# Kernel optimization log

Measured on AMD Instinct MI355X. Metric: run time of the kernel, lower is better.

The kernel has to match this reference:

```python
import jax, jax.numpy as jnp
import numpy as np

COST_W = {'cls': 1.0, 'center': 0.0, 'obj_ness': 0.0, 'giou': 2.0}
IOU_THRES = 0.25
MAX_DYN = 10
EPS = 1e-6
N_PRED, N_GT, N_CLS = 65536, 128, 256


def _to_bbox(centers, sizes):
    # center/size -> (x1,y1,z1,x2,y2,z2)
    return jnp.concatenate([centers - sizes / 2.0, centers + sizes / 2.0], axis=-1)


def _giou_3d(b1, b2):
    # b1 [N,6], b2 [M,6] -> giou [N,M] (axis_aligned_bbox_overlaps_3d, mode='giou')
    vol1 = jnp.prod(b1[:, 3:] - b1[:, :3], axis=-1)  # [N]
    vol2 = jnp.prod(b2[:, 3:] - b2[:, :3], axis=-1)  # [M]
    lt = jnp.maximum(b1[:, None, :3], b2[None, :, :3])  # [N,M,3]
    rb = jnp.minimum(b1[:, None, 3:], b2[None, :, 3:])
    overlap = jnp.prod(jnp.clip(rb - lt, 0.0), axis=-1)  # [N,M]
    union = jnp.maximum(vol1[:, None] + vol2[None, :] - overlap, EPS)
    iou = overlap / union
    elt = jnp.minimum(b1[:, None, :3], b2[None, :, :3])
    erb = jnp.maximum(b1[:, None, 3:], b2[None, :, 3:])
    enclose = jnp.maximum(jnp.prod(jnp.clip(erb - elt, 0.0), axis=-1), EPS)
    return iou - (enclose - union) / enclose


def _lsa(cost):
    # Jonker-Volgenant shortest-augmenting-path LAP (same optimum as
    # scipy.optimize.linear_sum_assignment). cost [n, m], n <= m.
    # Returns col4row[n]: column matched to each row.
    n, m = cost.shape
    u = np.zeros(n, np.float64)
    v = np.zeros(m, np.float64)
    col4row = np.full(n, -1, np.int64)
    row4col = np.full(m, -1, np.int64)
    cost = cost.astype(np.float64)
    for cur in range(n):
        shortest = np.full(m, np.inf)
        path = np.full(m, -1, np.int64)
        SC = np.zeros(m, bool)
        SR = []
        i, min_val, sink = cur, 0.0, -1
        while sink == -1:
            SR.append(i)
            r = min_val + cost[i] - u[i] - v
            upd = (~SC) & (r < shortest)
            shortest = np.where(upd, r, shortest)
            path = np.where(upd, i, path)
            masked = np.where(SC, np.inf, shortest)
            j = int(masked.argmin())
            min_val = masked[j]
            SC[j] = True
            if row4col[j] == -1:
                sink = j
            else:
                i = int(row4col[j])
        u[cur] += min_val
        for i2 in SR:
            if i2 != cur:
                u[i2] += min_val - shortest[col4row[i2]]
        v[SC] -= min_val - shortest[SC]
        j = sink
        while True:
            i2 = int(path[j])
            row4col[j] = i2
            col4row[i2], j = j, col4row[i2]
            if i2 == cur:
                break
    return col4row


def _dynamic_assign(giou, used0, order):
    # Sequential greedy IoU-threshold assignment over gts (ascending max-iou).
    NEG = jnp.float32(-1e9)
    n_pred = giou.shape[0]

    def step(used, gt_idx):
        col = giou[:, gt_idx]
        vals = jnp.where((col > IOU_THRES) & (~used), col, NEG)
        topv, topi = jax.lax.top_k(vals, MAX_DYN)
        valid = topv > NEG
        used = used | jnp.zeros((n_pred,), bool).at[topi].set(valid)
        return used, (jnp.where(valid, topi, -1), jnp.where(valid, gt_idx, -1))

    _, (dp, dg) = jax.lax.scan(step, used0, order)
    return dp.reshape(-1), dg.reshape(-1)  # padded with -1 where invalid


def setup_inputs() -> dict:
    key = jax.random.key(0)
    k = jax.random.split(key, 7)
    return {
        'all_centers': jax.random.normal(k[0], (N_PRED, 3), jnp.float32),
        'all_sizes': jax.random.uniform(k[1], (N_PRED, 3), jnp.float32),
        'all_cls': jax.random.normal(k[2], (N_PRED, N_CLS), jnp.float32),
        'all_objness': jax.random.normal(k[3], (N_PRED,), jnp.float32),
        'gt_centers': jax.random.normal(k[4], (N_GT, 3), jnp.float32),
        'gt_sizes': jax.random.uniform(k[5], (N_GT, 3), jnp.float32),
        'gt_labels': jax.random.randint(k[6], (N_GT,), 0, N_CLS, jnp.int64),
    }


def reference(all_centers, all_sizes, all_cls, all_objness, gt_centers, gt_sizes, gt_labels):
    pred_bbox = _to_bbox(all_centers, all_sizes)
    gt_bbox = _to_bbox(gt_centers, gt_sizes)
    giou = _giou_3d(pred_bbox, gt_bbox)  # [N, M]
    cost_class = -jax.nn.sigmoid(all_cls)[:, gt_labels]  # [N, M]
    cost_center = jnp.sum(jnp.abs(all_centers[:, None, :] - gt_centers[None, :, :]), axis=-1)  # cdist p=1
    cost_obj = -jax.nn.sigmoid(all_objness)[:, None]  # [N, 1]
    total_cost = (COST_W['cls'] * cost_class + COST_W['center'] * cost_center
                  + COST_W['obj_ness'] * cost_obj + COST_W['giou'] * (-giou))
    # Hungarian on transposed cost (M <= N): same optimal pairing as scipy on [N, M].
    col4row = _lsa(np.asarray(jax.device_get(total_cost)).T)
    pred_indices = jnp.asarray(col4row, jnp.int64)       # matched pred per gt
    gt_indices = jnp.arange(gt_labels.shape[0], dtype=jnp.int64)
    used0 = jnp.zeros((giou.shape[0],), bool).at[pred_indices].set(True)
    order = jnp.argsort(jnp.max(giou, axis=0))
    dp, dg = _dynamic_assign(giou, used0, order)
    combined_preds = jnp.concatenate([pred_indices, dp.astype(jnp.int64)])
    combined_gts = jnp.concatenate([gt_indices, dg.astype(jnp.int64)])
    return combined_preds, combined_gts
```

## Files before the change

### kernel.cpp

```cpp
#include <hip/hip_runtime.h>
#include <hip/hip_bf16.h>
#include <math.h>

#define NPRED 65536
#define NGT   128
#define NCLS  256
#define CAP   12288
#define VCAP  160
#define VSLOT 129
#define NLIST 129
#define LSTRIDE 132
#define KEEP  2048
#define KMIN  1418
#define GSPLIT 4
#define GPB   (NGT / GSPLIT)
#define SENT_I 0x7FFFFFFF


__device__ __forceinline__ unsigned f2u(float f) {
    unsigned u = __float_as_uint(f);
    return (u & 0x80000000u) ? ~u : (u | 0x80000000u);
}
__device__ __forceinline__ float u2f(unsigned x) {
    unsigned u = (x & 0x80000000u) ? (x ^ 0x80000000u) : ~x;
    return __uint_as_float(u);
}
__device__ __forceinline__ unsigned long long d2u(double d) {
    unsigned long long u = (unsigned long long)__double_as_longlong(d);
    return (u & 0x8000000000000000ull) ? ~u : (u | 0x8000000000000000ull);
}
__device__ __forceinline__ double u2d(unsigned long long x) {
    unsigned long long u = (x & 0x8000000000000000ull) ? (x ^ 0x8000000000000000ull) : ~x;
    return __longlong_as_double((long long)u);
}

__device__ __forceinline__ float giou3d(
    float pl0, float pl1, float pl2, float ph0, float ph1, float ph2, float pvol,
    float gl0, float gl1, float gl2, float gh0, float gh1, float gh2, float gvol)
{
#pragma clang fp contract(off)
    float c0 = fmaxf(fminf(ph0, gh0) - fmaxf(pl0, gl0), 0.0f);
    float c1 = fmaxf(fminf(ph1, gh1) - fmaxf(pl1, gl1), 0.0f);
    float c2 = fmaxf(fminf(ph2, gh2) - fmaxf(pl2, gl2), 0.0f);
    float overlap = (c0 * c1) * c2;
    float uni = fmaxf((pvol + gvol) - overlap, 1e-6f);
    float iou = overlap / uni;
    float e0 = fmaxf(fmaxf(ph0, gh0) - fminf(pl0, gl0), 0.0f);
    float e1 = fmaxf(fmaxf(ph1, gh1) - fminf(pl1, gl1), 0.0f);
    float e2 = fmaxf(fmaxf(ph2, gh2) - fminf(pl2, gl2), 0.0f);
    float enc = fmaxf((e0 * e1) * e2, 1e-6f);
    return iou - (enc - uni) / enc;
}


__global__ __launch_bounds__(256) void k_gather(
    const float* __restrict__ cls, const int* __restrict__ lab,
    float* __restrict__ costT,
    int* __restrict__ ccnt, unsigned* __restrict__ cmax, int* __restrict__ failFlag)
{
#pragma clang fp contract(off)
    __shared__ float tile[64][NCLS + 1];
    __shared__ int labl[NGT];
    int tid = threadIdx.x;
    int p0 = blockIdx.x * 64;
    if (blockIdx.x == 0) {
        if (tid < NGT) { ccnt[tid] = 0; cmax[tid] = 0u; }
        if (tid == 0) *failFlag = 0;
    }
    if (tid < NGT) labl[tid] = lab[tid];
    for (int it = 0; it < 16; ++it) {
        int row = it * 4 + (tid >> 6);
        int col = (tid & 63) * 4;
        const float4 v = *(const float4*)&cls[(size_t)(p0 + row) * NCLS + col];
        tile[row][col + 0] = v.x; tile[row][col + 1] = v.y;
        tile[row][col + 2] = v.z; tile[row][col + 3] = v.w;
    }
    __syncthreads();
    int lane = tid & 63;
    for (int rep = 0; rep < 32; ++rep) {
        int g = rep * 4 + (tid >> 6);
        float val = tile[lane][labl[g]];
        double s = 1.0 / (1.0 + exp(-(double)val));
        costT[(size_t)g * NPRED + p0 + lane] = -(float)s;
    }
}

__global__ __launch_bounds__(256) void k_cost(
    const float* __restrict__ pc, const float* __restrict__ ps,
    const float* __restrict__ gc, const float* __restrict__ gs,
    float* __restrict__ costT, int* __restrict__ ccnt, unsigned* __restrict__ cmax,
    int2* __restrict__ cpair)
{
#pragma clang fp contract(off)
    __shared__ float gb[GPB][6];
    __shared__ float gvol[GPB];
    __shared__ unsigned smax[GPB];
    __shared__ int cntl[GPB], basel[GPB], curl[GPB];
    int tid = threadIdx.x;
    int lane = tid & 63;
    int g0 = (blockIdx.x & (GSPLIT - 1)) * GPB;
    int p  = (blockIdx.x >> 2) * 256 + tid;

    if (tid < GPB) {
        int g = g0 + tid;
        float c0 = gc[g * 3 + 0], c1 = gc[g * 3 + 1], c2 = gc[g * 3 + 2];
        float s0 = gs[g * 3 + 0], s1 = gs[g * 3 + 1], s2 = gs[g * 3 + 2];
        float l0 = c0 - s0 / 2.0f, l1 = c1 - s1 / 2.0f, l2 = c2 - s2 / 2.0f;
        float h0 = c0 + s0 / 2.0f, h1 = c1 + s1 / 2.0f, h2 = c2 + s2 / 2.0f;
        gb[tid][0] = l0; gb[tid][1] = l1; gb[tid][2] = l2;
        gb[tid][3] = h0; gb[tid][4] = h1; gb[tid][5] = h2;
        gvol[tid] = ((h0 - l0) * (h1 - l1)) * (h2 - l2);
        smax[tid] = 0u; cntl[tid] = 0; curl[tid] = 0;
    }
    __syncthreads();

    float c0 = pc[p * 3 + 0], c1 = pc[p * 3 + 1], c2 = pc[p * 3 + 2];
    float s0 = ps[p * 3 + 0], s1 = ps[p * 3 + 1], s2 = ps[p * 3 + 2];
    float pl0 = c0 - s0 / 2.0f, pl1 = c1 - s1 / 2.0f, pl2 = c2 - s2 / 2.0f;
    float ph0 = c0 + s0 / 2.0f, ph1 = c1 + s1 / 2.0f, ph2 = c2 + s2 / 2.0f;
    float pvol = ((ph0 - pl0) * (ph1 - pl1)) * (ph2 - pl2);

    float gior[GPB];

#pragma unroll
    for (int gg = 0; gg < GPB; ++gg) {
        float gio = giou3d(pl0, pl1, pl2, ph0, ph1, ph2, pvol,
                           gb[gg][0], gb[gg][1], gb[gg][2], gb[gg][3], gb[gg][4], gb[gg][5],
                           gvol[gg]);
        gior[gg] = gio;
        float m = gio;
        for (int off = 32; off; off >>= 1) m = fmaxf(m, __shfl_xor(m, off, 64));
        unsigned long long mask = __ballot(gio > 0.25f);
        if (lane == 0) {
            atomicMax(&smax[gg], f2u(m));
            atomicAdd(&cntl[gg], __popcll(mask));
        }
        size_t ij = (size_t)(g0 + gg) * NPRED + p;
        float ns = costT[ij];
        costT[ij] = ns + (2.0f * (-gio));
    }
    __syncthreads();
    if (tid < GPB) {
        atomicMax(&cmax[g0 + tid], smax[tid]);
        basel[tid] = atomicAdd(&ccnt[g0 + tid], cntl[tid]);
    }
    __syncthreads();

#pragma unroll
    for (int gg = 0; gg < GPB; ++gg) {
        float gio = gior[gg];
        bool cand = (gio > 0.25f);
        unsigned long long mask = __ballot(cand);
        int cnt = __popcll(mask);
        int wo = 0;
        if (lane == 0 && cnt) wo = atomicAdd(&curl[gg], cnt);
        wo = __shfl(wo, 0, 64);
        if (cand) {
            int slot = basel[gg] + wo + __popcll(mask & ((1ull << lane) - 1ull));
            if (slot < CAP)
                cpair[(size_t)(g0 + gg) * CAP + slot] = make_int2(p, __float_as_int(gio));
        }
    }
}

__global__ __launch_bounds__(256) void k_toprow(
    const float* __restrict__ costT, int2* __restrict__ rowlist,
    const unsigned* __restrict__ cmax, int* __restrict__ order)
{
    __shared__ unsigned long long keys[2048];
    __shared__ int hist[256];
    __shared__ unsigned long long sh_prefix;
    __shared__ int sh_rank, sh_cnt, sh_ok;
    __shared__ unsigned msort[NGT];
    int tid = threadIdx.x;
    int row = blockIdx.x;

    if (row == NGT) {
        if (tid < NGT) msort[tid] = cmax[tid];
        __syncthreads();
        if (tid < NGT) {
            unsigned mt = msort[tid];
            int r = 0;
            for (int k = 0; k < NGT; ++k) {
                unsigned mk = msort[k];
                if (mk < mt || (mk == mt && k < tid)) r++;
            }
            order[r] = tid;
        }
        return;
    }
    const float* crow = costT + (size_t)row * NPRED;

    unsigned long long lv[8];
#pragma unroll
    for (int q = 0; q < 8; ++q) lv[q] = ~0ull;
    const float4* crow4 = (const float4*)crow;
    for (int it = tid; it < NPRED / 4; it += 256) {
        float4 v4 = crow4[it];
        int j = it * 4;
        float vv[4] = {v4.x, v4.y, v4.z, v4.w};
#pragma unroll
        for (int e = 0; e < 4; ++e) {
            unsigned long long key =
                ((unsigned long long)f2u(vv[e]) << 32) | (unsigned)(j + e);
            if (key < lv[7]) {
                unsigned long long c = key;
#pragma unroll
                for (int q = 0; q < 8; ++q) {
                    unsigned long long mx = (c > lv[q]) ? c : lv[q];
                    unsigned long long mn = (c > lv[q]) ? lv[q] : c;
                    lv[q] = mn; c = mx;
                }
            }
        }
    }
#pragma unroll
    for (int q = 0; q < 8; ++q) keys[tid * 8 + q] = lv[q];
    if (tid == 0) sh_ok = 1;
    __syncthreads();

    for (int k = 2; k <= 2048; k <<= 1) {
        for (int j2 = k >> 1; j2 > 0; j2 >>= 1) {
            for (int i = tid; i < 2048; i += 256) {
                int ixj = i ^ j2;
                if (ixj > i) {
                    unsigned long long a = keys[i], b2 = keys[ixj];
                    bool up = ((i & k) == 0);
                    if ((up && a > b2) || (!up && a < b2)) { keys[i] = b2; keys[ixj] = a; }
                }
            }
            __syncthreads();
        }
    }

    unsigned long long thr = keys[NLIST - 1];
    if (lv[7] < thr) sh_ok = 0;
    __syncthreads();

    if (sh_ok) {
        if (tid < NLIST) {
            unsigned long long key = keys[tid];
            rowlist[row * LSTRIDE + tid] =
                make_int2(__float_as_int(u2f((unsigned)(key >> 32))),
                          (int)(unsigned)(key & 0xFFFFFFFFull));
        }
        return;
    }

    if (tid == 0) { sh_prefix = 0ull; sh_rank = NLIST - 1; sh_cnt = 0; }
    __syncthreads();
    for (int d = 7; d >= 0; --d) {
        hist[tid] = 0;
        __syncthreads();
        unsigned long long pref = sh_prefix;
        int sh = (d + 1) * 8;
        for (int j = tid; j < NPRED; j += 256) {
            unsigned long long key = ((unsigned long long)f2u(crow[j]) << 32) | (unsigned)j;
            bool match = (sh >= 64) || ((key >> sh) == (pref >> sh));
            if (match) atomicAdd(&hist[(int)((key >> (d * 8)) & 255ull)], 1);
        }
        __syncthreads();
        if (tid == 0) {
            int rank = sh_rank, cum = 0, b = 0;
            for (; b < 256; ++b) { if (cum + hist[b] > rank) break; cum += hist[b]; }
            sh_prefix = pref | ((unsigned long long)b << (d * 8));
            sh_rank = rank - cum;
        }
        __syncthreads();
    }
    unsigned long long thr2 = sh_prefix;
    for (int j = tid; j < NPRED; j += 256) {
        unsigned long long key = ((unsigned long long)f2u(crow[j]) << 32) | (unsigned)j;
        if (key <= thr2) { int s = atomicAdd(&sh_cnt, 1); keys[s] = key; }
    }
    __syncthreads();
    if (tid >= sh_cnt) keys[tid] = ~0ull;
    __syncthreads();
    for (int k = 2; k <= 256; k <<= 1) {
        for (int j2 = k >> 1; j2 > 0; j2 >>= 1) {
            int i = tid, ixj = i ^ j2;
            if (ixj > i) {
                unsigned long long a = keys[i], b2 = keys[ixj];
                bool up = ((i & k) == 0);
                if ((up && a > b2) || (!up && a < b2)) { keys[i] = b2; keys[ixj] = a; }
            }
            __syncthreads();
        }
    }
    if (tid < NLIST) {
        unsigned long long key = keys[tid];
        rowlist[row * LSTRIDE + tid] =
            make_int2(__float_as_int(u2f((unsigned)(key >> 32))),
                      (int)(unsigned)(key & 0xFFFFFFFFull));
    }
}

__global__ __launch_bounds__(64) void k_lsa_sparse(
    const float* __restrict__ costT, const int2* __restrict__ rowlist,
    int* __restrict__ failFlag,
    unsigned* __restrict__ usedbits, int* __restrict__ out)
{
#pragma clang fp contract(off)
    __shared__ float  costV[NGT][VSLOT];
    __shared__ double u_l[NGT];
    __shared__ int    c4r[NGT];
    __shared__ int    slot4row[NGT];
    __shared__ int    headpos[NGT];
    __shared__ int    colidV[VCAP];
    __shared__ int    pathV[VCAP], r4cV[VCAP];
    __shared__ int    SRr[VCAP];
    __shared__ double headv[VCAP];
    __shared__ int    headj[VCAP];
    __shared__ unsigned vbits[2048];

    int lane = threadIdx.x;
    for (int w = lane; w < 2048; w += 64) vbits[w] = 0u;
    for (int r = lane; r < NGT; r += 64) {
        u_l[r] = 0.0; c4r[r] = -1; slot4row[r] = -1; headpos[r] = 0;
    }
    double short0 = INFINITY, short1 = INFINITY;
    double v0 = 0.0, v1 = 0.0;
    int col0 = SENT_I, col1 = SENT_I;
    int sc0 = 0, sc1 = 0;
    int nV = 0;
    bool fail = false;
    __syncthreads();

    for (int cur = 0; cur < NGT && !fail; ++cur) {
        short0 = INFINITY; short1 = INFINITY; sc0 = 0; sc1 = 0;
        if (lane < nV)      pathV[lane]      = -1;
        if (lane + 64 < nV) pathV[lane + 64] = -1;
        if (lane == 0) SRr[0] = cur;
        int bi = cur, s = 1, pendrow = cur, pendpos = 0, sink = -1;
        double mv = 0.0, pendmv = 0.0;
        __syncthreads();
        int pos = headpos[cur];
        int i0 = pos + lane;
        int2 e0 = (i0 < NLIST) ? rowlist[cur * LSTRIDE + i0] : make_int2(0, SENT_I);

        while (true) {
            int prow = pendrow;
            int pp   = pendpos;
            double pmv = pendmv;

            double ui = u_l[bi];
            unsigned long long bvk = ~0ull, btk = ~0ull;
            if (lane < nV && !sc0) {
                double c = (double)costV[bi][lane];
                double r = ((mv + c) - ui) - v0;
                if (r < short0) { short0 = r; pathV[lane] = bi; }
                unsigned long long vk = d2u(short0);
                unsigned long long tk = ((unsigned long long)(unsigned)col0 << 32)
                                        | (0x80000000u | (unsigned)lane);
                if (vk < bvk || (vk == bvk && tk < btk)) { bvk = vk; btk = tk; }
            }
            int k1 = lane + 64;
            if (k1 < nV && !sc1) {
                double c = (double)costV[bi][k1];
                double r = ((mv + c) - ui) - v1;
                if (r < short1) { short1 = r; pathV[k1] = bi; }
                unsigned long long vk = d2u(short1);
                unsigned long long tk = ((unsigned long long)(unsigned)col1 << 32)
                                        | (0x80000000u | (unsigned)k1);
                if (vk < bvk || (vk == bvk && tk < btk)) { bvk = vk; btk = tk; }
            }
            for (int p = lane; p < s; p += 64) {
                if (p == pp) continue;
                unsigned long long vk = d2u(headv[p]);
                unsigned long long tk = ((unsigned long long)(unsigned)headj[p] << 32)
                                        | (unsigned)p;
                if (vk < bvk || (vk == bvk && tk < btk)) { bvk = vk; btk = tk; }
            }

            int hcol = SENT_I; float hval = 0.0f;
            {
                int c0 = e0.y;
                bool fresh = (i0 < NLIST) && !((vbits[c0 >> 5] >> (c0 & 31)) & 1u);
                unsigned long long m0 = __ballot(fresh);
                if (m0) {
                    int fl = __ffsll(m0) - 1;
                    hcol = __shfl(c0, fl, 64);
                    hval = __shfl(__int_as_float(e0.x), fl, 64);
                    pos += fl;
                } else {
                    pos += 64;
                    while (pos < NLIST) {
                        int i = pos + lane;
                        int2 e = (i < NLIST) ? rowlist[prow * LSTRIDE + i] : make_int2(0, SENT_I);
                        int c = e.y;
                        bool fr = (i < NLIST) && !((vbits[c >> 5] >> (c & 31)) & 1u);
                        unsigned long long m = __ballot(fr);
                        if (m) {
                            int fl = __ffsll(m) - 1;
                            hcol = __shfl(c, fl, 64);
                            hval = __shfl(__int_as_float(e.x), fl, 64);
                            pos += fl;
                            break;
                        }
                        pos += 64;
                    }
                }
            }
            double pend_headv = (hcol == SENT_I) ? (double)INFINITY
                                : ((pmv + (double)hval) - u_l[prow]);
            {
                unsigned long long vk = d2u(pend_headv);
                unsigned long long tk = ((unsigned long long)(unsigned)hcol << 32)
                                        | (unsigned)pp;
                if (vk < bvk || (vk == bvk && tk < btk)) { bvk = vk; btk = tk; }
            }

#pragma unroll
            for (int off = 1; off < 64; off <<= 1) {
                unsigned long long ov = __shfl_xor(bvk, off, 64);
                unsigned long long ot = __shfl_xor(btk, off, 64);
                if (ov < bvk || (ov == bvk && ot < btk)) { bvk = ov; btk = ot; }
            }
            double bv = u2d(bvk);
            unsigned tlow = (unsigned)btk;
            int bj   = (int)(btk >> 32);
            int bisv = (int)(tlow >> 31);
            int baux = (int)(tlow & 0x7FFFFFFFu);
            mv = bv;

            if (lane == 0) {
                headpos[prow] = pos;
                headv[pp] = pend_headv; headj[pp] = hcol;
            }
            if (bisv) {
                if ((baux & 63) == lane) {
                    if (baux & 64) sc1 = 1; else sc0 = 1;
                }
                int nr = r4cV[baux];
                if (lane == 0) SRr[s] = nr;
                pendrow = nr; pendpos = s; pendmv = bv; bi = nr; ++s;
                pos = headpos[nr];
                i0 = pos + lane;
                e0 = (i0 < NLIST) ? rowlist[nr * LSTRIDE + i0] : make_int2(0, SENT_I);
                __syncthreads();
            } else {
                if (nV >= VCAP) {
                    fail = true;
                } else {
                    if ((nV & 63) == lane) {
                        if (nV & 64) { col1 = bj; v1 = 0.0; short1 = bv; sc1 = 1; }
                        else         { col0 = bj; v0 = 0.0; short0 = bv; sc0 = 1; }
                    }
                    if (lane == 0) {
                        colidV[nV] = bj;
                        pathV[nV] = SRr[baux]; r4cV[nV] = -1;
                        vbits[bj >> 5] |= (1u << (bj & 31));
                    }
                    sink = bj;
                    ++nV;
                }
                __syncthreads();
                break;
            }
        }
        if (fail) break;

        int snew = nV - 1;
        float pfa = costT[(size_t)lane * NPRED + sink];
        float pfb = costT[(size_t)(lane + 64) * NPRED + sink];

        double mvf = mv;
        if (lane < nV && sc0)      v0 -= (mvf - short0);
        if (lane + 64 < nV && sc1) v1 -= (mvf - short1);

        {
            int q = lane;
            bool act = (q >= 1 && q < s);
            int i2 = act ? SRr[q] : 0;
            int sl = act ? slot4row[i2] : 0;
            double gA = __shfl(short0, sl & 63, 64);
            double gB = __shfl(short1, sl & 63, 64);
            double sv = (sl & 64) ? gB : gA;
            if (act) u_l[i2] += mvf - sv;
        }
        {
            int q = lane + 64;
            bool act = (q >= 1 && q < s);
            int i2 = act ? SRr[q] : 0;
            int sl = act ? slot4row[i2] : 0;
            double gA = __shfl(short0, sl & 63, 64);
            double gB = __shfl(short1, sl & 63, 64);
            double sv = (sl & 64) ? gB : gA;
            if (act) u_l[i2] += mvf - sv;
        }
        if (lane == 0) u_l[cur] += mvf;

        if (lane == 0) {
            int jslot = snew;
            while (true) {
                int i2 = pathV[jslot];
                r4cV[jslot] = i2;
                int oldslot = (c4r[i2] >= 0) ? slot4row[i2] : -1;
                c4r[i2] = colidV[jslot];
                slot4row[i2] = jslot;
                if (i2 == cur) break;
                jslot = oldslot;
            }
        }
        costV[lane][snew]      = pfa;
        costV[lane + 64][snew] = pfb;
        __syncthreads();
    }

    if (lane == 0 && fail) *failFlag = 1;
    __syncthreads();
    if (!fail) {
        for (int w = lane; w < 2048; w += 64) usedbits[w] = 0u;
        __syncthreads();
        for (int r = lane; r < NGT; r += 64) {
            int p = c4r[r];
            atomicOr(&usedbits[p >> 5], 1u << (p & 31));
            out[r] = p;
            out[1408 + r] = r;
        }
    }
}

__global__ __launch_bounds__(1024) void k_lsa_dense(
    const float* __restrict__ costT, const int* __restrict__ failFlag,
    double* __restrict__ v, double* __restrict__ shortest,
    int* __restrict__ path, int* __restrict__ row4col,
    unsigned char* __restrict__ SC, unsigned* __restrict__ usedbits,
    int* __restrict__ out)
{
#pragma clang fp contract(off)
    if (*failFlag == 0) return;
    __shared__ double u_l[NGT];
    __shared__ int    c4r[NGT];
    __shared__ int    SR[NGT + 1];
    __shared__ int    bi, bsink, nSR;
    __shared__ double bmin;
    __shared__ double wval[16];
    __shared__ int    widx[16];
    int tid = threadIdx.x;

    for (int j = tid; j < NPRED; j += 1024) { v[j] = 0.0; row4col[j] = -1; }
    if (tid < NGT) { u_l[tid] = 0.0; c4r[tid] = -1; }
    __syncthreads();

    for (int cur = 0; cur < NGT; ++cur) {
        for (int j = tid; j < NPRED; j += 1024) {
            shortest[j] = (double)INFINITY; path[j] = -1; SC[j] = 0;
        }
        if (tid == 0) { bi = cur; bsink = -1; bmin = 0.0; SR[0] = cur; nSR = 1; }
        __syncthreads();

        while (true) {
            int irow = bi;
            double mv = bmin;
            double ui = u_l[irow];
            const float* crow = costT + (size_t)irow * NPRED;
            double bestv = (double)INFINITY;
            int    bestj = SENT_I;
            for (int j = tid; j < NPRED; j += 1024) {
                if (!SC[j]) {
                    double s = shortest[j];
                    double r = ((mv + (double)crow[j]) - ui) - v[j];
                    if (r < s) { s = r; shortest[j] = r; path[j] = irow; }
                    if (s < bestv || (s == bestv && j < bestj)) { bestv = s; bestj = j; }
                }
            }
            for (int off = 32; off; off >>= 1) {
                double ov = __shfl_down(bestv, off, 64);
                int    oj = __shfl_down(bestj, off, 64);
                if (ov < bestv || (ov == bestv && oj < bestj)) { bestv = ov; bestj = oj; }
            }
            if ((tid & 63) == 0) { wval[tid >> 6] = bestv; widx[tid >> 6] = bestj; }
            __syncthreads();
            if (tid == 0) {
                double bv = wval[0]; int bj = widx[0];
                for (int w = 1; w < 16; ++w) {
                    double ov = wval[w]; int oj = widx[w];
                    if (ov < bv || (ov == bv && oj < bj)) { bv = ov; bj = oj; }
                }
                bmin = bv;
                SC[bj] = 1;
                int r = row4col[bj];
                if (r < 0) { bsink = bj; }
                else       { SR[nSR++] = r; bi = r; }
            }
            __syncthreads();
            if (bsink >= 0) break;
        }

        double mv = bmin;
        for (int j = tid; j < NPRED; j += 1024)
            if (SC[j]) v[j] -= (mv - shortest[j]);
        if (tid == 0) {
            u_l[cur] += mv;
            for (int k = 1; k < nSR; ++k) {
                int i2 = SR[k];
                u_l[i2] += mv - shortest[c4r[i2]];
            }
            int j = bsink;
            while (true) {
                int i2 = path[j];
                row4col[j] = i2;
                int nj = c4r[i2];
                c4r[i2] = j;
                j = nj;
                if (i2 == cur) break;
            }
        }
        __syncthreads();
    }

    for (int w = tid; w < 2048; w += 1024) usedbits[w] = 0u;
    __syncthreads();
    for (int j = tid; j < NPRED; j += 1024)
        if (row4col[j] >= 0) atomicOr(&usedbits[j >> 5], 1u << (j & 31));
    if (tid < NGT) {
        out[tid]        = c4r[tid];
        out[1408 + tid] = tid;
    }
}

__global__ __launch_bounds__(256) void k_prep(
    const int2* __restrict__ cpair, const int* __restrict__ ccnt,
    unsigned long long* __restrict__ scand, int* __restrict__ kcount,
    int* __restrict__ fullflag)
{
    __shared__ int hist[256];
    __shared__ unsigned long long keys[KEEP];
    __shared__ unsigned sh_pref, sh_thresh;
    __shared__ int sh_done, sh_fail, sh_cnt;
    int tid = threadIdx.x;
    int g = blockIdx.x;
    int nc = ccnt[g]; if (nc > CAP) nc = CAP;
    const int2* src = cpair + (size_t)g * CAP;

    unsigned thresh = 0;
    if (nc > KEEP - 1) {
        if (tid == 0) { sh_pref = 0; sh_done = 0; sh_fail = 0; }
        __syncthreads();
        int above = 0;
        for (int byt = 3; byt >= 0; --byt) {
            hist[tid] = 0;
            __syncthreads();
            unsigned pref = sh_pref;
            for (int c = tid; c < nc; c += 256) {
                unsigned u = f2u(__int_as_float(src[c].y));
                if (byt == 3 || (u >> ((byt + 1) * 8)) == (pref >> ((byt + 1) * 8)))
                    atomicAdd(&hist[(u >> (byt * 8)) & 255], 1);
            }
            __syncthreads();
            if (tid == 0) {
                int cum = 0, B = 0, kept = 0, abnew = above;
                for (int b = 255; b >= 0; --b) {
                    if (above + cum + hist[b] >= KMIN) {
                        B = b; kept = above + cum + hist[b]; abnew = above + cum; break;
                    }
                    cum += hist[b];
                }
                if (kept <= KEEP - 1) { sh_thresh = sh_pref | ((unsigned)B << (byt * 8)); sh_done = 1; }
                else {
                    above = abnew;
                    sh_pref = sh_pref | ((unsigned)B << (byt * 8));
                    if (byt == 0) sh_fail = 1;
                }
            }
            __syncthreads();
            if (sh_done || sh_fail) break;
        }
        if (sh_fail) {
            if (tid == 0) { fullflag[g] = 1; kcount[g] = 0; }
            return;
        }
        thresh = sh_thresh;
    }
    if (tid == 0) sh_cnt = 0;
    __syncthreads();
    for (int c = tid; c < nc; c += 256) {
        unsigned u = f2u(__int_as_float(src[c].y));
        if (u >= thresh) {
            int slot = atomicAdd(&sh_cnt, 1);
            keys[slot] = ((unsigned long long)(~u) << 32) | (unsigned)src[c].x;
        }
    }
    __syncthreads();
    int kept = sh_cnt;
    for (int i = tid; i < KEEP; i += 256) if (i >= kept) keys[i] = ~0ull;
    __syncthreads();
    for (int k = 2; k <= KEEP; k <<= 1) {
        for (int j = k >> 1; j > 0; j >>= 1) {
            for (int i = tid; i < KEEP; i += 256) {
                int ixj = i ^ j;
                if (ixj > i) {
                    unsigned long long a = keys[i], b = keys[ixj];
                    bool up = ((i & k) == 0);
                    if ((up && a > b) || (!up && a < b)) { keys[i] = b; keys[ixj] = a; }
                }
            }
            __syncthreads();
        }
    }
    for (int i = tid; i < KEEP; i += 256) scand[(size_t)g * KEEP + i] = keys[i];
    if (tid == 0) { kcount[g] = kept; fullflag[g] = 0; }
}

__global__ __launch_bounds__(64) void k_dyn2(
    const int* __restrict__ order, const int* __restrict__ kcount,
    const unsigned long long* __restrict__ scand, const int* __restrict__ fullflag,
    const int* __restrict__ ccnt, const int2* __restrict__ cpair,
    const unsigned* __restrict__ usedbits_g, const int* __restrict__ failFlag,
    int* __restrict__ out)
{
    __shared__ unsigned bits[2048];
    int lane = threadIdx.x;
    for (int w = lane; w < 2048; w += 64) bits[w] = usedbits_g[w];
    __syncthreads();
    bool globalFull = (*failFlag != 0);

    for (int k = 0; k < NGT; ++k) {
        int gt = order[k];
        int got = 0;
        if (!globalFull && fullflag[gt] == 0) {
            int kept = kcount[gt];
            int base = 0;
            while (got < 10 && base < kept) {
                int i = base + lane;
                unsigned long long key = (i < kept) ? scand[(size_t)gt * KEEP + i] : ~0ull;
                int p = (int)(unsigned)(key & 0xFFFFFFFFull);
                bool ok = (key != ~0ull) && !((bits[p >> 5] >> (p & 31)) & 1u);
                unsigned long long mask = __ballot(ok);
                int need = 10 - got;
                int pre = __popcll(mask & ((1ull << lane) - 1ull));
                if (ok && pre < need) {
                    out[128 + k * 10 + got + pre] = p;
                    out[1408 + 128 + k * 10 + got + pre] = gt;
                    atomicOr(&bits[p >> 5], 1u << (p & 31));
                }
                int tot = __popcll(mask);
                got += (tot < need) ? tot : need;
                base += 64;
                __syncthreads();
            }
        } else {
            int nc = ccnt[gt]; if (nc > CAP) nc = CAP;
            float lv[10]; int li[10];
#pragma unroll
            for (int q = 0; q < 10; ++q) { lv[q] = -1e30f; li[q] = SENT_I; }
            for (int c = lane; c < nc; c += 64) {
                int2 pr = cpair[(size_t)gt * CAP + c];
                int p = pr.x;
                if ((bits[p >> 5] >> (p & 31)) & 1u) continue;
                float cv = __int_as_float(pr.y); int ci = p;
#pragma unroll
                for (int q = 0; q < 10; ++q) {
                    bool b = (cv > lv[q]) || (cv == lv[q] && ci < li[q]);
                    float tv = b ? lv[q] : cv; int ti = b ? li[q] : ci;
                    if (b) { lv[q] = cv; li[q] = ci; }
                    cv = tv; ci = ti;
                }
            }
#pragma unroll
            for (int q = 0; q < 10; ++q) {
                float mo = lv[0]; int mj = li[0];
#pragma unroll
                for (int off = 1; off < 64; off <<= 1) {
                    float ov = __shfl_xor(mo, off, 64);
                    int oj = __shfl_xor(mj, off, 64);
                    if (ov > mo || (ov == mo && oj < mj)) { mo = ov; mj = oj; }
                }
                bool valid = (mj != SENT_I);
                if (valid && li[0] == mj) {
#pragma unroll
                    for (int t = 0; t < 9; ++t) { lv[t] = lv[t + 1]; li[t] = li[t + 1]; }
                    lv[9] = -1e30f; li[9] = SENT_I;
                }
                if (lane == q) {
                    out[128 + k * 10 + q] = valid ? mj : -1;
                    out[1408 + 128 + k * 10 + q] = valid ? gt : -1;
                    if (valid) atomicOr(&bits[mj >> 5], 1u << (mj & 31));
                }
            }
            got = 10;
            __syncthreads();
        }
        for (int q = got + lane; q < 10; q += 64) {
            out[128 + k * 10 + q] = -1;
            out[1408 + 128 + k * 10 + q] = -1;
        }
        __syncthreads();
    }
}


extern "C" void kernel_launch(void* const* d_in, const int* in_sizes, int n_in,
                              void* d_out, int out_size, void* d_ws, size_t ws_size,
                              hipStream_t stream) {
    const float* pc  = (const float*)d_in[0];
    const float* ps  = (const float*)d_in[1];
    const float* cls = (const float*)d_in[2];
    const float* gc  = (const float*)d_in[4];
    const float* gs  = (const float*)d_in[5];
    const int*   lab = (const int*)d_in[6];

    char* ws = (char*)d_ws;
    float*         costT    = (float*)(ws + 0);
    unsigned long long* scand = (unsigned long long*)(ws + 0);
    int2*          rowlist  = (int2*)(ws + 33554432);
    double*        v        = (double*)(ws + 33554432);
    double*        shortest = (double*)(ws + 34078720);
    int*           path     = (int*)(ws + 34603008);
    int*           row4col  = (int*)(ws + 34865152);
    unsigned char* SC       = (unsigned char*)(ws + 35127296);
    int*           kcount   = (int*)(ws + 35192832);
    int*           fullflag = (int*)(ws + 35193344);
    int*           ccnt     = (int*)(ws + 35193856);
    unsigned*      cmax     = (unsigned*)(ws + 35194368);
    int*           order    = (int*)(ws + 35194880);
    int*           failFlag = (int*)(ws + 35195392);
    unsigned*      usedbits = (unsigned*)(ws + 35195904);
    int2*          cpair    = (int2*)(ws + 35204096);

    int* out = (int*)d_out;

    hipLaunchKernelGGL(k_gather, dim3(NPRED / 64), dim3(256), 0, stream,
                       cls, lab, costT, ccnt, cmax, failFlag);
    hipLaunchKernelGGL(k_cost, dim3((NPRED / 256) * GSPLIT), dim3(256), 0, stream,
                       pc, ps, gc, gs, costT, ccnt, cmax, cpair);
    hipLaunchKernelGGL(k_toprow, dim3(NGT + 1), dim3(256), 0, stream,
                       costT, rowlist, cmax, order);
    hipLaunchKernelGGL(k_lsa_sparse, dim3(1), dim3(64), 0, stream,
                       costT, rowlist, failFlag, usedbits, out);
    hipLaunchKernelGGL(k_lsa_dense, dim3(1), dim3(1024), 0, stream,
                       costT, failFlag, v, shortest, path, row4col, SC, usedbits, out);
    hipLaunchKernelGGL(k_prep, dim3(NGT), dim3(256), 0, stream,
                       cpair, ccnt, scand, kcount, fullflag);
    hipLaunchKernelGGL(k_dyn2, dim3(1), dim3(64), 0, stream,
                       order, kcount, scand, fullflag, ccnt, cpair, usedbits, failFlag, out);
}
```

Measured before the change: 690.3 us.

## Replace bitonic sort in top-row selection with radix select over candidates

k_toprow now runs with 512 threads, each keeping its 8 smallest keys, so there are 4096 candidates in shared memory. The full 2048-key bitonic sort is replaced by an 8-pass radix histogram select over those candidates to find the 129th-smallest threshold. Keys at or below the threshold are compacted into a 256-entry buffer, which is then bitonic-sorted. The fallback full-row radix select is kept for the case where a thread's local list may have overflowed. The aim is to cut sort synchronisation and shared-memory traffic in exchange for eight rounds of histogram atomics; with 129 blocks on a large GPU, occupancy and parallelism also change.

```diff
diff --git a/kernel.cpp b/kernel.cpp
--- a/kernel.cpp
+++ b/kernel.cpp
@@ -14,6 +14,7 @@
 #define KMIN  1418
 #define GSPLIT 4
 #define GPB   (NGT / GSPLIT)
+#define NCAND 4096
 #define SENT_I 0x7FFFFFFF
 
 
@@ -163,11 +164,12 @@
     }
 }
 
-__global__ __launch_bounds__(256) void k_toprow(
+__global__ __launch_bounds__(512) void k_toprow(
     const float* __restrict__ costT, int2* __restrict__ rowlist,
     const unsigned* __restrict__ cmax, int* __restrict__ order)
 {
-    __shared__ unsigned long long keys[2048];
+    __shared__ unsigned long long keys[NCAND];
+    __shared__ unsigned long long cbuf[256];
     __shared__ int hist[256];
     __shared__ unsigned long long sh_prefix;
     __shared__ int sh_rank, sh_cnt, sh_ok;
@@ -190,14 +192,12 @@
         return;
     }
     const float* crow = costT + (size_t)row * NPRED;
+    const float4* crow4 = (const float4*)crow;
 
     unsigned long long lv[8];
 #pragma unroll
     for (int q = 0; q < 8; ++q) lv[q] = ~0ull;
-    const float4* crow4 = (const float4*)crow;
-    for (int it = tid; it < NPRED / 4; it += 256) {
-        float4 v4 = crow4[it];
-        int j = it * 4;
+    auto ins4 = [&](float4 v4, int j) {
         float vv[4] = {v4.x, v4.y, v4.z, v4.w};
 #pragma unroll
         for (int e = 0; e < 4; ++e) {
@@ -213,49 +213,29 @@
                 }
             }
         }
+    };
+    for (int base = 0; base < 32; base += 4) {
+        float4 va = crow4[tid + (base + 0) * 512];
+        float4 vb = crow4[tid + (base + 1) * 512];
+        float4 vc = crow4[tid + (base + 2) * 512];
+        float4 vd = crow4[tid + (base + 3) * 512];
+        ins4(va, (tid + (base + 0) * 512) * 4);
+        ins4(vb, (tid + (base + 1) * 512) * 4);
+        ins4(vc, (tid + (base + 2) * 512) * 4);
+        ins4(vd, (tid + (base + 3) * 512) * 4);
     }
 #pragma unroll
     for (int q = 0; q < 8; ++q) keys[tid * 8 + q] = lv[q];
-    if (tid == 0) sh_ok = 1;
-    __syncthreads();
-
-    for (int k = 2; k <= 2048; k <<= 1) {
-        for (int j2 = k >> 1; j2 > 0; j2 >>= 1) {
-            for (int i = tid; i < 2048; i += 256) {
-                int ixj = i ^ j2;
-                if (ixj > i) {
-                    unsigned long long a = keys[i], b2 = keys[ixj];
-                    bool up = ((i & k) == 0);
-                    if ((up && a > b2) || (!up && a < b2)) { keys[i] = b2; keys[ixj] = a; }
-                }
-            }
-            __syncthreads();
-        }
-    }
-
-    unsigned long long thr = keys[NLIST - 1];
-    if (lv[7] < thr) sh_ok = 0;
-    __syncthreads();
-
-    if (sh_ok) {
-        if (tid < NLIST) {
-            unsigned long long key = keys[tid];
-            rowlist[row * LSTRIDE + tid] =
-                make_int2(__float_as_int(u2f((unsigned)(key >> 32))),
-                          (int)(unsigned)(key & 0xFFFFFFFFull));
-        }
-        return;
-    }
-
-    if (tid == 0) { sh_prefix = 0ull; sh_rank = NLIST - 1; sh_cnt = 0; }
-    __syncthreads();
+    if (tid == 0) { sh_ok = 1; sh_prefix = 0ull; sh_rank = NLIST - 1; sh_cnt = 0; }
+    __syncthreads();
+
     for (int d = 7; d >= 0; --d) {
-        hist[tid] = 0;
+        if (tid < 256) hist[tid] = 0;
         __syncthreads();
         unsigned long long pref = sh_prefix;
         int sh = (d + 1) * 8;
-        for (int j = tid; j < NPRED; j += 256) {
-            unsigned long long key = ((unsigned long long)f2u(crow[j]) << 32) | (unsigned)j;
+        for (int i = tid; i < NCAND; i += 512) {
+            unsigned long long key = keys[i];
             bool match = (sh >= 64) || ((key >> sh) == (pref >> sh));
             if (match) atomicAdd(&hist[(int)((key >> (d * 8)) & 255ull)], 1);
         }
@@ -268,27 +248,65 @@
         }
         __syncthreads();
     }
-    unsigned long long thr2 = sh_prefix;
-    for (int j = tid; j < NPRED; j += 256) {
-        unsigned long long key = ((unsigned long long)f2u(crow[j]) << 32) | (unsigned)j;
-        if (key <= thr2) { int s = atomicAdd(&sh_cnt, 1); keys[s] = key; }
-    }
-    __syncthreads();
-    if (tid >= sh_cnt) keys[tid] = ~0ull;
+    unsigned long long t = sh_prefix;
+    if (lv[7] < t) sh_ok = 0;
+    __syncthreads();
+    bool ok = (sh_ok != 0);
+
+    if (ok) {
+        for (int i = tid; i < NCAND; i += 512) {
+            unsigned long long key = keys[i];
+            if (key <= t) { int s2 = atomicAdd(&sh_cnt, 1); cbuf[s2] = key; }
+        }
+        __syncthreads();
+    } else {
+        if (tid == 0) { sh_prefix = 0ull; sh_rank = NLIST - 1; sh_cnt = 0; }
+        __syncthreads();
+        for (int d = 7; d >= 0; --d) {
+            if (tid < 256) hist[tid] = 0;
+            __syncthreads();
+            unsigned long long pref = sh_prefix;
+            int sh = (d + 1) * 8;
+            for (int j = tid; j < NPRED; j += 512) {
+                unsigned long long key = ((unsigned long long)f2u(crow[j]) << 32) | (unsigned)j;
+                bool match = (sh >= 64) || ((key >> sh) == (pref >> sh));
+                if (match) atomicAdd(&hist[(int)((key >> (d * 8)) & 255ull)], 1);
+            }
+            __syncthreads();
+            if (tid == 0) {
+                int rank = sh_rank, cum = 0, b = 0;
+                for (; b < 256; ++b) { if (cum + hist[b] > rank) break; cum += hist[b]; }
+                sh_prefix = pref | ((unsigned long long)b << (d * 8));
+                sh_rank = rank - cum;
+            }
+            __syncthreads();
+        }
+        unsigned long long thr2 = sh_prefix;
+        for (int j = tid; j < NPRED; j += 512) {
+            unsigned long long key = ((unsigned long long)f2u(crow[j]) << 32) | (unsigned)j;
+            if (key <= thr2) { int s2 = atomicAdd(&sh_cnt, 1); cbuf[s2] = key; }
+        }
+        __syncthreads();
+    }
+
+    int kept = sh_cnt;
+    if (tid < 256 && tid >= kept) cbuf[tid] = ~0ull;
     __syncthreads();
     for (int k = 2; k <= 256; k <<= 1) {
         for (int j2 = k >> 1; j2 > 0; j2 >>= 1) {
-            int i = tid, ixj = i ^ j2;
-            if (ixj > i) {
-                unsigned long long a = keys[i], b2 = keys[ixj];
-                bool up = ((i & k) == 0);
-                if ((up && a > b2) || (!up && a < b2)) { keys[i] = b2; keys[ixj] = a; }
+            if (tid < 256) {
+                int i = tid, ixj = i ^ j2;
+                if (ixj > i) {
+                    unsigned long long a = cbuf[i], b2 = cbuf[ixj];
+                    bool up = ((i & k) == 0);
+                    if ((up && a > b2) || (!up && a < b2)) { cbuf[i] = b2; cbuf[ixj] = a; }
+                }
             }
             __syncthreads();
         }
     }
     if (tid < NLIST) {
-        unsigned long long key = keys[tid];
+        unsigned long long key = cbuf[tid];
         rowlist[row * LSTRIDE + tid] =
             make_int2(__float_as_int(u2f((unsigned)(key >> 32))),
                       (int)(unsigned)(key & 0xFFFFFFFFull));
@@ -825,7 +843,7 @@
                        cls, lab, costT, ccnt, cmax, failFlag);
     hipLaunchKernelGGL(k_cost, dim3((NPRED / 256) * GSPLIT), dim3(256), 0, stream,
                        pc, ps, gc, gs, costT, ccnt, cmax, cpair);
-    hipLaunchKernelGGL(k_toprow, dim3(NGT + 1), dim3(256), 0, stream,
+    hipLaunchKernelGGL(k_toprow, dim3(NGT + 1), dim3(512), 0, stream,
                        costT, rowlist, cmax, order);
     hipLaunchKernelGGL(k_lsa_sparse, dim3(1), dim3(64), 0, stream,
                        costT, rowlist, failFlag, usedbits, out);
```

Result: faster. 662.8 us (-4.0%).
